# Optimization experiments

Hardware: AMD Instinct MI355X
Metric: run time of the kernel (lower is better)

The kernel has to match this reference:

```python
import jax, jax.numpy as jnp
import numpy as np

COUPLING = 1.0
DT = 1.0
ATTRACTION = 1.0
EPS = 1e-6


def setup_inputs() -> dict:
    key = jax.random.key(0)
    k1, k2, k3, k4 = jax.random.split(key, 4)
    B, N, D = 4, 2048, 4
    theta_prev = jax.random.normal(k1, (B, N, D), dtype=jnp.float32)
    gamma_prev = jax.random.normal(k2, (B, N, D), dtype=jnp.float32)
    theta_connectivity_weight = jax.random.uniform(k3, (B, N, N), dtype=jnp.float32)
    alpha_t = jax.random.normal(k4, (B, N, N), dtype=jnp.float32)
    return {
        "theta_prev": theta_prev,
        "gamma_prev": gamma_prev,
        "theta_connectivity_weight": theta_connectivity_weight,
        "alpha_t": alpha_t,
    }


def reference(theta_prev, gamma_prev, theta_connectivity_weight, alpha_t):
    # Pairwise coupling: coupling/N * sum_j W[b,i,j] * sin(theta[b,j,d] - theta[b,i,d] - alpha[b,i,j])
    # Expanded via trig identities so the O(N^2*D) tensor is never materialized:
    #   sin(tj - ti - a) = cos(a)*(s_j c_i - c_j s_i) - sin(a)*(c_j c_i + s_j s_i)
    # => sum_j W_ij sin(...) = c_i*(A s)_i - s_i*(A c)_i - c_i*(Bm c)_i - s_i*(Bm s)_i
    # with A = W*cos(alpha), Bm = W*sin(alpha). This matches the chunked torch loop exactly.
    n = theta_prev.shape[1]
    s = jnp.sin(theta_prev)  # [B, N, D]
    c = jnp.cos(theta_prev)  # [B, N, D]
    A = theta_connectivity_weight * jnp.cos(alpha_t)   # [B, N, N]
    Bm = theta_connectivity_weight * jnp.sin(alpha_t)  # [B, N, N]
    As = jnp.einsum("bij,bjd->bid", A, s)
    Ac = jnp.einsum("bij,bjd->bid", A, c)
    Bs = jnp.einsum("bij,bjd->bid", Bm, s)
    Bc = jnp.einsum("bij,bjd->bid", Bm, c)
    coupling_term = (COUPLING / n) * (c * As - s * Ac - c * Bc - s * Bs)
    drive_term = ATTRACTION * (gamma_prev - theta_prev)
    theta_next = theta_prev + DT * (drive_term + coupling_term)
    # torch F.normalize: x / clamp(||x||_2, min=eps) along last dim
    norm = jnp.linalg.norm(theta_next, axis=-1, keepdims=True)
    return theta_next / jnp.maximum(norm, EPS)
```

## Files before the change

### kernel.cpp

```cpp
#include <hip/hip_runtime.h>
#include <stdint.h>

#define N_NODES 2048
#define N_BATCH 4
#define ROWS_PER_BLOCK 8
#define THREADS 512

__device__ __forceinline__ uint32_t bf16rn(float x) {
    uint32_t u = __float_as_uint(x);
    u += 0x7fffu + ((u >> 16) & 1u);
    return u >> 16;
}

__global__ __launch_bounds__(THREADS, 8) void kuramoto_kernel(
    const float* __restrict__ theta,
    const float* __restrict__ gamma,
    const float* __restrict__ W,
    const float* __restrict__ alpha,
    float* __restrict__ out)
{
    __shared__ uint4 table[N_NODES];

    const int tid  = threadIdx.x;
    const int lane = tid & 63;
    const int wave = tid >> 6;
    const int b    = blockIdx.x >> 8;
    const int i    = ((blockIdx.x & 255) * ROWS_PER_BLOCK) + wave;

    const float* thb = theta + (size_t)b * (N_NODES * 4);
    #pragma unroll
    for (int g = 0; g < N_NODES / THREADS; ++g) {
        const int j = tid + g * THREADS;
        const float4 u = *(const float4*)(thb + (size_t)j * 4);
        const float th[4] = {u.x, u.y, u.z, u.w};
        uint32_t p[4];
        #pragma unroll
        for (int d = 0; d < 4; ++d) {
            float s, c;
            __sincosf(th[d], &s, &c);
            p[d] = (bf16rn(c) << 16) | bf16rn(s);
        }
        table[j] = make_uint4(p[0], p[1], p[2], p[3]);
    }
    __syncthreads();

    const size_t rowbase = ((size_t)b * N_NODES + i) * N_NODES;
    const float* Wr = W + rowbase;
    const float* Ar = alpha + rowbase;

    float re[4] = {0.f, 0.f, 0.f, 0.f};
    float im[4] = {0.f, 0.f, 0.f, 0.f};

    #pragma unroll 8
    for (int it = 0; it < N_NODES / 64; ++it) {
        const int j = it * 64 + lane;
        const float w = Wr[j];
        const float a = Ar[j];
        float sa, ca;
        __sincosf(a, &sa, &ca);
        const float A  = w * ca;
        const float Bq = w * sa;
        const uint4 t = table[j];
        const uint32_t tw[4] = {t.x, t.y, t.z, t.w};
        #pragma unroll
        for (int d = 0; d < 4; ++d) {
            const float s = __uint_as_float(tw[d] << 16);
            const float c = __uint_as_float(tw[d] & 0xffff0000u);
            re[d] = fmaf(A,  c, re[d]);
            re[d] = fmaf(Bq, s, re[d]);
            im[d] = fmaf(A,  s, im[d]);
            im[d] = fmaf(-Bq, c, im[d]);
        }
    }

    #pragma unroll
    for (int stage = 1; stage < 64; stage <<= 1) {
        #pragma unroll
        for (int d = 0; d < 4; ++d) {
            re[d] += __shfl_xor(re[d], stage, 64);
            im[d] += __shfl_xor(im[d], stage, 64);
        }
    }

    if (lane == 0) {
        const size_t obase = ((size_t)b * N_NODES + i) * 4;
        const float4 th4 = *(const float4*)(thb + (size_t)i * 4);
        const float4 g4  = *(const float4*)(gamma + obase);
        const float thd[4] = {th4.x, th4.y, th4.z, th4.w};
        const float gd[4]  = {g4.x, g4.y, g4.z, g4.w};
        float t[4];
        float s2 = 0.0f;
        #pragma unroll
        for (int d = 0; d < 4; ++d) {
            float s_i, c_i;
            __sincosf(thd[d], &s_i, &c_i);
            const float coup = (c_i * im[d] - s_i * re[d]) * (1.0f / (float)N_NODES);
            t[d] = gd[d] + coup;
            s2 = fmaf(t[d], t[d], s2);
        }
        const float inv = 1.0f / fmaxf(sqrtf(s2), 1e-6f);
        *(float4*)(out + obase) = make_float4(t[0]*inv, t[1]*inv, t[2]*inv, t[3]*inv);
    }
}

extern "C" void kernel_launch(void* const* d_in, const int* in_sizes, int n_in,
                              void* d_out, int out_size, void* d_ws, size_t ws_size,
                              hipStream_t stream) {
    const float* theta = (const float*)d_in[0];
    const float* gamma = (const float*)d_in[1];
    const float* W     = (const float*)d_in[2];
    const float* alpha = (const float*)d_in[3];
    float* out = (float*)d_out;

    const int grid = (N_BATCH * N_NODES) / ROWS_PER_BLOCK;
    hipLaunchKernelGGL(kuramoto_kernel, dim3(grid), dim3(THREADS), 0, stream,
                       theta, gamma, W, alpha, out);
}
```

Before: 156.7 us.

## Vectorize W/alpha loads to float4 with register prefetch and SoA LDS table

Each lane now loads four consecutive W and alpha elements as float4 instead of one float per iteration, and the next chunk is prefetched into registers while the current one is computed. The first chunk's load is issued before the LDS table build so it overlaps the sin/cos setup. The shared table becomes dimension-major (SoA) so each lane reads four consecutive j entries per dimension with 128-bit LDS loads. This aims to cut global load instruction count and hide memory latency, at the cost of more registers per thread, which could reduce occupancy.

Result: slower. 165.7 us (+5.7%).

```diff
diff --git a/kernel.cpp b/kernel.cpp
--- a/kernel.cpp
+++ b/kernel.cpp
@@ -19,7 +19,7 @@
     const float* __restrict__ alpha,
     float* __restrict__ out)
 {
-    __shared__ uint4 table[N_NODES];
+    __shared__ uint32_t tbl[4][N_NODES];
 
     const int tid  = threadIdx.x;
     const int lane = tid & 63;
@@ -27,50 +27,74 @@
     const int b    = blockIdx.x >> 8;
     const int i    = ((blockIdx.x & 255) * ROWS_PER_BLOCK) + wave;
 
+    const size_t rowbase = ((size_t)b * N_NODES + i) * N_NODES;
+    const float* Wr = W + rowbase;
+    const float* Ar = alpha + rowbase;
+
+    const int jfirst = lane * 4;
+    float4 wc = *(const float4*)(Wr + jfirst);
+    float4 ac = *(const float4*)(Ar + jfirst);
+
     const float* thb = theta + (size_t)b * (N_NODES * 4);
     #pragma unroll
     for (int g = 0; g < N_NODES / THREADS; ++g) {
         const int j = tid + g * THREADS;
         const float4 u = *(const float4*)(thb + (size_t)j * 4);
         const float th[4] = {u.x, u.y, u.z, u.w};
-        uint32_t p[4];
         #pragma unroll
         for (int d = 0; d < 4; ++d) {
             float s, c;
             __sincosf(th[d], &s, &c);
-            p[d] = (bf16rn(c) << 16) | bf16rn(s);
+            tbl[d][j] = (bf16rn(c) << 16) | bf16rn(s);
         }
-        table[j] = make_uint4(p[0], p[1], p[2], p[3]);
     }
     __syncthreads();
-
-    const size_t rowbase = ((size_t)b * N_NODES + i) * N_NODES;
-    const float* Wr = W + rowbase;
-    const float* Ar = alpha + rowbase;
 
     float re[4] = {0.f, 0.f, 0.f, 0.f};
     float im[4] = {0.f, 0.f, 0.f, 0.f};
 
-    #pragma unroll 8
-    for (int it = 0; it < N_NODES / 64; ++it) {
-        const int j = it * 64 + lane;
-        const float w = Wr[j];
-        const float a = Ar[j];
-        float sa, ca;
-        __sincosf(a, &sa, &ca);
-        const float A  = w * ca;
-        const float Bq = w * sa;
-        const uint4 t = table[j];
-        const uint32_t tw[4] = {t.x, t.y, t.z, t.w};
+    #pragma unroll
+    for (int it = 0; it < N_NODES / 256; ++it) {
+        const int j0 = it * 256 + lane * 4;
+
+        const uint4 t0 = *(const uint4*)&tbl[0][j0];
+        const uint4 t1 = *(const uint4*)&tbl[1][j0];
+        const uint4 t2 = *(const uint4*)&tbl[2][j0];
+        const uint4 t3 = *(const uint4*)&tbl[3][j0];
+
+        float4 wn, an;
+        if (it < N_NODES / 256 - 1) {
+            wn = *(const float4*)(Wr + j0 + 256);
+            an = *(const float4*)(Ar + j0 + 256);
+        }
+
+        const float wq[4] = {wc.x, wc.y, wc.z, wc.w};
+        const float aq[4] = {ac.x, ac.y, ac.z, ac.w};
+        float A[4], Bq[4];
+        #pragma unroll
+        for (int q = 0; q < 4; ++q) {
+            float sa, ca;
+            __sincosf(aq[q], &sa, &ca);
+            A[q]  = wq[q] * ca;
+            Bq[q] = wq[q] * sa;
+        }
+
         #pragma unroll
         for (int d = 0; d < 4; ++d) {
-            const float s = __uint_as_float(tw[d] << 16);
-            const float c = __uint_as_float(tw[d] & 0xffff0000u);
-            re[d] = fmaf(A,  c, re[d]);
-            re[d] = fmaf(Bq, s, re[d]);
-            im[d] = fmaf(A,  s, im[d]);
-            im[d] = fmaf(-Bq, c, im[d]);
+            const uint4 t = (d == 0) ? t0 : (d == 1) ? t1 : (d == 2) ? t2 : t3;
+            const uint32_t tu[4] = {t.x, t.y, t.z, t.w};
+            #pragma unroll
+            for (int q = 0; q < 4; ++q) {
+                const float s = __uint_as_float(tu[q] << 16);
+                const float c = __uint_as_float(tu[q] & 0xffff0000u);
+                re[d] = fmaf(A[q],   c, re[d]);
+                re[d] = fmaf(Bq[q],  s, re[d]);
+                im[d] = fmaf(A[q],   s, im[d]);
+                im[d] = fmaf(-Bq[q], c, im[d]);
+            }
         }
+
+        if (it < N_NODES / 256 - 1) { wc = wn; ac = an; }
     }
 
     #pragma unroll
```

## Vectorize row loads to float4, transpose sin/cos table, prefetch next chunk

Applied to the files above, without the earlier changes.

Each lane now loads four consecutive W and alpha values as float4 instead of one scalar per iteration. The shared sin/cos table is transposed to a per-dimension layout so each lane reads a uint4 of four consecutive nodes per dimension. The first chunk is loaded before the table build, and each loop iteration prefetches the next 256-column chunk into registers before consuming the current one, overlapping global latency with the FMA work. The loop is no longer unrolled, so memory-level parallelism depends on this software prefetch, and register use rises.

After: 151.0 us (median of 2 runs). -3.6%, faster.

```diff
diff --git a/kernel.cpp b/kernel.cpp
--- a/kernel.cpp
+++ b/kernel.cpp
@@ -19,7 +19,7 @@
     const float* __restrict__ alpha,
     float* __restrict__ out)
 {
-    __shared__ uint4 table[N_NODES];
+    __shared__ uint32_t tbl[4][N_NODES];
 
     const int tid  = threadIdx.x;
     const int lane = tid & 63;
@@ -27,51 +27,70 @@
     const int b    = blockIdx.x >> 8;
     const int i    = ((blockIdx.x & 255) * ROWS_PER_BLOCK) + wave;
 
+    const size_t rowbase = ((size_t)b * N_NODES + i) * N_NODES;
+    const float* Wr = W + rowbase;
+    const float* Ar = alpha + rowbase;
+
+    const int jfirst = lane * 4;
+    float4 wc = *(const float4*)(Wr + jfirst);
+    float4 ac = *(const float4*)(Ar + jfirst);
+
     const float* thb = theta + (size_t)b * (N_NODES * 4);
     #pragma unroll
     for (int g = 0; g < N_NODES / THREADS; ++g) {
         const int j = tid + g * THREADS;
         const float4 u = *(const float4*)(thb + (size_t)j * 4);
         const float th[4] = {u.x, u.y, u.z, u.w};
-        uint32_t p[4];
         #pragma unroll
         for (int d = 0; d < 4; ++d) {
             float s, c;
             __sincosf(th[d], &s, &c);
-            p[d] = (bf16rn(c) << 16) | bf16rn(s);
+            tbl[d][j] = (bf16rn(c) << 16) | bf16rn(s);
         }
-        table[j] = make_uint4(p[0], p[1], p[2], p[3]);
     }
     __syncthreads();
-
-    const size_t rowbase = ((size_t)b * N_NODES + i) * N_NODES;
-    const float* Wr = W + rowbase;
-    const float* Ar = alpha + rowbase;
 
     float re[4] = {0.f, 0.f, 0.f, 0.f};
     float im[4] = {0.f, 0.f, 0.f, 0.f};
 
-    #pragma unroll 8
-    for (int it = 0; it < N_NODES / 64; ++it) {
-        const int j = it * 64 + lane;
-        const float w = Wr[j];
-        const float a = Ar[j];
-        float sa, ca;
-        __sincosf(a, &sa, &ca);
-        const float A  = w * ca;
-        const float Bq = w * sa;
-        const uint4 t = table[j];
-        const uint32_t tw[4] = {t.x, t.y, t.z, t.w};
-        #pragma unroll
-        for (int d = 0; d < 4; ++d) {
-            const float s = __uint_as_float(tw[d] << 16);
-            const float c = __uint_as_float(tw[d] & 0xffff0000u);
-            re[d] = fmaf(A,  c, re[d]);
-            re[d] = fmaf(Bq, s, re[d]);
-            im[d] = fmaf(A,  s, im[d]);
-            im[d] = fmaf(-Bq, c, im[d]);
-        }
+    #define CONSUME(WV, AV, J0)                                              \
+    do {                                                                     \
+        const float wq_[4] = {(WV).x, (WV).y, (WV).z, (WV).w};               \
+        const float aq_[4] = {(AV).x, (AV).y, (AV).z, (AV).w};               \
+        float A_[4], Bq_[4];                                                 \
+        _Pragma("unroll")                                                    \
+        for (int q = 0; q < 4; ++q) {                                        \
+            float sa_, ca_;                                                  \
+            __sincosf(aq_[q], &sa_, &ca_);                                   \
+            A_[q]  = wq_[q] * ca_;                                           \
+            Bq_[q] = wq_[q] * sa_;                                           \
+        }                                                                    \
+        _Pragma("unroll")                                                    \
+        for (int d = 0; d < 4; ++d) {                                        \
+            const uint4 t_ = *(const uint4*)&tbl[d][(J0)];   \
+            const uint32_t tu_[4] = {t_.x, t_.y, t_.z, t_.w};                \
+            _Pragma("unroll")                                                \
+            for (int q = 0; q < 4; ++q) {                                    \
+                const float s_ = __uint_as_float(tu_[q] << 16);              \
+                const float c_ = __uint_as_float(tu_[q] & 0xffff0000u);      \
+                re[d] = fmaf(A_[q],   c_, re[d]);                            \
+                re[d] = fmaf(Bq_[q],  s_, re[d]);                            \
+                im[d] = fmaf(A_[q],   s_, im[d]);                            \
+                im[d] = fmaf(-Bq_[q], c_, im[d]);                            \
+            }                                                                \
+        }                                                                    \
+    } while (0)
+
+    #pragma unroll 1
+    for (int it = 0; it < N_NODES / 256 - 1; ++it) {
+        const int j0 = it * 256 + lane * 4;
+        const float4 wn = *(const float4*)(Wr + j0 + 256);
+        const float4 an = *(const float4*)(Ar + j0 + 256);
+        CONSUME(wc, ac, j0);
+        wc = wn; ac = an;
     }
+    CONSUME(wc, ac, (N_NODES / 256 - 1) * 256 + lane * 4);
+    #undef CONSUME
 
     #pragma unroll
     for (int stage = 1; stage < 64; stage <<= 1) {
```

## Precompute sin/cos table in separate kernel and map one row per block

Applied to the files above, without the earlier changes.

Moves the per-node sin/cos bf16 table out of each block's shared memory into a small prologue kernel that writes it to the workspace, so blocks no longer recompute all 2048 entries. The main kernel now gives each 256-thread block one row, with each thread issuing float4 loads of 8 contiguous W/alpha elements, and reads table entries from global memory or cache. The per-row reduction becomes a shuffle stage plus a cross-wave shared-memory reduction. The output step also uses bf16 sin/cos of theta_i from the table instead of full-precision values, which lowers accuracy. It adds a second launch and uncoalesced per-thread table reads.

Measured after the change: 186.1 us. +18.7%, slower.

```diff
diff --git a/kernel.cpp b/kernel.cpp
--- a/kernel.cpp
+++ b/kernel.cpp
@@ -3,8 +3,6 @@
 
 #define N_NODES 2048
 #define N_BATCH 4
-#define ROWS_PER_BLOCK 8
-#define THREADS 512
 
 __device__ __forceinline__ uint32_t bf16rn(float x) {
     uint32_t u = __float_as_uint(x);
@@ -12,64 +10,77 @@
     return u >> 16;
 }
 
-__global__ __launch_bounds__(THREADS, 8) void kuramoto_kernel(
-    const float* __restrict__ theta,
+__global__ __launch_bounds__(256) void table_kernel(
+    const float* __restrict__ theta, uint4* __restrict__ tbl)
+{
+    const int idx = blockIdx.x * 256 + threadIdx.x;
+    const float4 u = *(const float4*)(theta + (size_t)idx * 4);
+    const float th[4] = {u.x, u.y, u.z, u.w};
+    uint32_t p[4];
+    #pragma unroll
+    for (int d = 0; d < 4; ++d) {
+        float s, c;
+        __sincosf(th[d], &s, &c);
+        p[d] = (bf16rn(c) << 16) | bf16rn(s);
+    }
+    tbl[idx] = make_uint4(p[0], p[1], p[2], p[3]);
+}
+
+__global__ __launch_bounds__(256, 8) void kuramoto_kernel(
     const float* __restrict__ gamma,
     const float* __restrict__ W,
     const float* __restrict__ alpha,
+    const uint4* __restrict__ tbl,
     float* __restrict__ out)
 {
-    __shared__ uint4 table[N_NODES];
+    __shared__ float red[4][8];
 
     const int tid  = threadIdx.x;
     const int lane = tid & 63;
     const int wave = tid >> 6;
-    const int b    = blockIdx.x >> 8;
-    const int i    = ((blockIdx.x & 255) * ROWS_PER_BLOCK) + wave;
-
-    const float* thb = theta + (size_t)b * (N_NODES * 4);
-    #pragma unroll
-    for (int g = 0; g < N_NODES / THREADS; ++g) {
-        const int j = tid + g * THREADS;
-        const float4 u = *(const float4*)(thb + (size_t)j * 4);
-        const float th[4] = {u.x, u.y, u.z, u.w};
-        uint32_t p[4];
-        #pragma unroll
-        for (int d = 0; d < 4; ++d) {
-            float s, c;
-            __sincosf(th[d], &s, &c);
-            p[d] = (bf16rn(c) << 16) | bf16rn(s);
-        }
-        table[j] = make_uint4(p[0], p[1], p[2], p[3]);
-    }
-    __syncthreads();
+    const int b = blockIdx.x >> 11;
+    const int i = blockIdx.x & (N_NODES - 1);
 
     const size_t rowbase = ((size_t)b * N_NODES + i) * N_NODES;
-    const float* Wr = W + rowbase;
-    const float* Ar = alpha + rowbase;
+    const int j0 = tid * 8;
+
+    const float4 w0 = *(const float4*)(W     + rowbase + j0);
+    const float4 w1 = *(const float4*)(W     + rowbase + j0 + 4);
+    const float4 a0 = *(const float4*)(alpha + rowbase + j0);
+    const float4 a1 = *(const float4*)(alpha + rowbase + j0 + 4);
+
+    const uint4* tb = tbl + ((size_t)b * N_NODES + j0);
 
     float re[4] = {0.f, 0.f, 0.f, 0.f};
     float im[4] = {0.f, 0.f, 0.f, 0.f};
 
-    #pragma unroll 8
-    for (int it = 0; it < N_NODES / 64; ++it) {
-        const int j = it * 64 + lane;
-        const float w = Wr[j];
-        const float a = Ar[j];
-        float sa, ca;
-        __sincosf(a, &sa, &ca);
-        const float A  = w * ca;
-        const float Bq = w * sa;
-        const uint4 t = table[j];
-        const uint32_t tw[4] = {t.x, t.y, t.z, t.w};
+    #pragma unroll
+    for (int h = 0; h < 2; ++h) {
+        const float4 wv = h ? w1 : w0;
+        const float4 av = h ? a1 : a0;
+        const uint4 t0 = tb[h * 4 + 0];
+        const uint4 t1 = tb[h * 4 + 1];
+        const uint4 t2 = tb[h * 4 + 2];
+        const uint4 t3 = tb[h * 4 + 3];
+        const float wq[4] = {wv.x, wv.y, wv.z, wv.w};
+        const float aq[4] = {av.x, av.y, av.z, av.w};
         #pragma unroll
-        for (int d = 0; d < 4; ++d) {
-            const float s = __uint_as_float(tw[d] << 16);
-            const float c = __uint_as_float(tw[d] & 0xffff0000u);
-            re[d] = fmaf(A,  c, re[d]);
-            re[d] = fmaf(Bq, s, re[d]);
-            im[d] = fmaf(A,  s, im[d]);
-            im[d] = fmaf(-Bq, c, im[d]);
+        for (int q = 0; q < 4; ++q) {
+            float sa, ca;
+            __sincosf(aq[q], &sa, &ca);
+            const float A  = wq[q] * ca;
+            const float Bq = wq[q] * sa;
+            const uint4 t = (q == 0) ? t0 : (q == 1) ? t1 : (q == 2) ? t2 : t3;
+            const uint32_t tu[4] = {t.x, t.y, t.z, t.w};
+            #pragma unroll
+            for (int d = 0; d < 4; ++d) {
+                const float s = __uint_as_float(tu[d] << 16);
+                const float c = __uint_as_float(tu[d] & 0xffff0000u);
+                re[d] = fmaf(A,   c, re[d]);
+                re[d] = fmaf(Bq,  s, re[d]);
+                im[d] = fmaf(A,   s, im[d]);
+                im[d] = fmaf(-Bq, c, im[d]);
+            }
         }
     }
 
@@ -81,20 +92,34 @@
             im[d] += __shfl_xor(im[d], stage, 64);
         }
     }
+    if (lane == 0) {
+        #pragma unroll
+        for (int d = 0; d < 4; ++d) {
+            red[wave][d]     = re[d];
+            red[wave][4 + d] = im[d];
+        }
+    }
+    __syncthreads();
 
-    if (lane == 0) {
+    if (tid == 0) {
+        float R[4], I[4];
+        #pragma unroll
+        for (int d = 0; d < 4; ++d) {
+            R[d] = red[0][d]     + red[1][d]     + red[2][d]     + red[3][d];
+            I[d] = red[0][4 + d] + red[1][4 + d] + red[2][4 + d] + red[3][4 + d];
+        }
         const size_t obase = ((size_t)b * N_NODES + i) * 4;
-        const float4 th4 = *(const float4*)(thb + (size_t)i * 4);
-        const float4 g4  = *(const float4*)(gamma + obase);
-        const float thd[4] = {th4.x, th4.y, th4.z, th4.w};
-        const float gd[4]  = {g4.x, g4.y, g4.z, g4.w};
+        const uint4 ti = tbl[(size_t)b * N_NODES + i];
+        const uint32_t tiu[4] = {ti.x, ti.y, ti.z, ti.w};
+        const float4 g4 = *(const float4*)(gamma + obase);
+        const float gd[4] = {g4.x, g4.y, g4.z, g4.w};
         float t[4];
         float s2 = 0.0f;
         #pragma unroll
         for (int d = 0; d < 4; ++d) {
-            float s_i, c_i;
-            __sincosf(thd[d], &s_i, &c_i);
-            const float coup = (c_i * im[d] - s_i * re[d]) * (1.0f / (float)N_NODES);
+            const float s_i = __uint_as_float(tiu[d] << 16);
+            const float c_i = __uint_as_float(tiu[d] & 0xffff0000u);
+            const float coup = (c_i * I[d] - s_i * R[d]) * (1.0f / (float)N_NODES);
             t[d] = gd[d] + coup;
             s2 = fmaf(t[d], t[d], s2);
         }
@@ -111,8 +136,10 @@
     const float* W     = (const float*)d_in[2];
     const float* alpha = (const float*)d_in[3];
     float* out = (float*)d_out;
+    uint4* tbl = (uint4*)d_ws;
 
-    const int grid = (N_BATCH * N_NODES) / ROWS_PER_BLOCK;
-    hipLaunchKernelGGL(kuramoto_kernel, dim3(grid), dim3(THREADS), 0, stream,
-                       theta, gamma, W, alpha, out);
+    hipLaunchKernelGGL(table_kernel, dim3((N_BATCH * N_NODES) / 256), dim3(256),
+                       0, stream, theta, tbl);
+    hipLaunchKernelGGL(kuramoto_kernel, dim3(N_BATCH * N_NODES), dim3(256),
+                       0, stream, gamma, W, alpha, tbl, out);
 }
```
